# Optimization experiments

Hardware: AMD Instinct MI355X
Metric: run time of the kernel (lower is better)

## Reference

```python
import jax, jax.numpy as jnp
import numpy as np

BINS = 15
STEPS = 25
BETA = 0.8
THR = 1.0
ALPHA = 2.0  # snntorch surrogate.atan default
B = 131072
NUM_FEATURES = 4  # 60 / 15 bins


@jax.custom_vjp
def spike_fn(x):
    # Heaviside on shifted membrane (mem - threshold)
    return (x > 0).astype(x.dtype)


def _spike_fwd(x):
    return spike_fn(x), x


def _spike_bwd(x, g):
    # snntorch ATan surrogate gradient: alpha/2 / (1 + (pi/2 * alpha * x)^2)
    return (g * (ALPHA / 2) / (1 + (jnp.pi / 2 * ALPHA * x) ** 2),)


spike_fn.defvjp(_spike_fwd, _spike_bwd)


def population_encode(x, bins=BINS):
    # vectorized equivalent of the scalar double loop: one-hot bucketing per feature
    x = jnp.clip(x, 0.0, 1.0)
    idx = jnp.clip((x * (bins - 1)).astype(jnp.int32), 0, bins - 1)  # [B, F]
    bsz, nfeat = x.shape
    return jax.nn.one_hot(idx, bins, dtype=x.dtype).reshape(bsz, nfeat * bins)  # [B, F*bins]


def setup_inputs() -> dict:
    key = jax.random.key(0)
    k0, k1, k2, k3, k4 = jax.random.split(key, 5)
    x = jax.random.uniform(k0, (B, NUM_FEATURES), dtype=jnp.float32)
    # fc1: Linear(60, 64); fc2: Linear(64, 3). torch layout: W [out, in]
    s1 = 1.0 / np.sqrt(60.0)
    s2 = 1.0 / np.sqrt(64.0)
    W1 = jax.random.uniform(k1, (64, 60), jnp.float32, -s1, s1)
    b1 = jax.random.uniform(k2, (64,), jnp.float32, -s1, s1)
    W2 = jax.random.uniform(k3, (3, 64), jnp.float32, -s2, s2)
    b2 = jax.random.uniform(k4, (3,), jnp.float32, -s2, s2)
    return {"x": x, "W1": W1, "b1": b1, "W2": W2, "b2": b2}


def reference(x, W1, b1, W2, b2):
    x_pop = population_encode(x)                # [B, 60]
    cur1 = x_pop @ W1.T + b1                    # [B, 64]; constant over steps (fc1 recomputed on same input)
    mem1_0 = jnp.zeros_like(cur1)               # [B, 64]
    mem2_0 = jnp.zeros((x.shape[0], W2.shape[0]), cur1.dtype)  # [B, 3]

    def step(carry, _):
        mem1, mem2 = carry
        # snntorch Leaky: reset from spike of incoming mem (detached), then leak+integrate, then fire
        reset1 = jax.lax.stop_gradient((mem1 > THR).astype(mem1.dtype))
        mem1 = BETA * mem1 + cur1 - reset1 * THR
        spk1 = spike_fn(mem1 - THR)
        cur2 = spk1 @ W2.T + b2                 # [B, 3]
        reset2 = jax.lax.stop_gradient((mem2 > THR).astype(mem2.dtype))
        mem2 = BETA * mem2 + cur2 - reset2 * THR
        spk2 = spike_fn(mem2 - THR)
        return (mem1, mem2), (spk2, spk1)

    _, (spk2_rec, spk1_rec) = jax.lax.scan(step, (mem1_0, mem2_0), None, length=STEPS)
    return spk2_rec, spk1_rec, x_pop            # [25,B,3], [25,B,64], [B,60]
```

## Files before the change

### kernel.cpp

```cpp
#include <hip/hip_runtime.h>


#define BINS   15
#define STEPS  25
#define NH     64
#define NO     3
#define NF     4
#define TPB    256

typedef float f32x4 __attribute__((ext_vector_type(4)));

__global__ __launch_bounds__(TPB) void popnet_kernel(
                              const float* __restrict__ x,
                              const float* __restrict__ W1,
                              const float* __restrict__ b1,
                              const float* __restrict__ W2,
                              const float* __restrict__ b2,
                              float* __restrict__ out, int B)
{
    __shared__ float W1s[NH * 60];
    __shared__ float b1s[NH];
    __shared__ float W2s[NO * NH];
    __shared__ float b2s[NO];
    __shared__ unsigned long long s1bits[TPB];
    __shared__ float s2f[TPB * NO];
    __shared__ unsigned int idxs[TPB];

    const int tid = threadIdx.x;
    for (int i = tid; i < NH * 60; i += TPB) W1s[i] = W1[i];
    for (int i = tid; i < NH;      i += TPB) b1s[i] = b1[i];
    for (int i = tid; i < NO * NH; i += TPB) W2s[i] = W2[i];
    if (tid < NO) b2s[tid] = b2[tid];
    __syncthreads();

    const int blockStart = blockIdx.x * TPB;
    const int b = blockStart + tid;

    const f32x4 xv = *reinterpret_cast<const f32x4*>(x + (size_t)b * NF);
    int idx[NF];
#pragma unroll
    for (int f = 0; f < NF; ++f) {
        float v = fminf(fmaxf(xv[f], 0.0f), 1.0f);
        int id = (int)(v * 14.0f);
        id = min(max(id, 0), BINS - 1);
        idx[f] = id;
    }
    idxs[tid] = (unsigned)idx[0] | ((unsigned)idx[1] << 4) |
                ((unsigned)idx[2] << 8) | ((unsigned)idx[3] << 12);
    const int c0 = idx[0], c1 = 15 + idx[1], c2 = 30 + idx[2], c3 = 45 + idx[3];

    float cur1[NH];
#pragma unroll
    for (int o = 0; o < NH; ++o) {
        const float* row = W1s + o * 60;
        float s = __fadd_rn(__fadd_rn(__fadd_rn(row[c0], row[c1]), row[c2]), row[c3]);
        cur1[o] = __fadd_rn(s, b1s[o]);
    }

    float mem1[NH];
#pragma unroll
    for (int o = 0; o < NH; ++o) mem1[o] = 0.0f;
    float mem2[NO] = {0.0f, 0.0f, 0.0f};

    const size_t off1 = (size_t)STEPS * B * NO;
    const size_t off2 = off1 + (size_t)STEPS * B * NH;
    float* const out_spk2 = out;
    float* const out_spk1 = out + off1;
    float* const out_xpop = out + off2;

#pragma unroll 1
    for (int t = 0; t < STEPS; ++t) {
        float acc0 = 0.0f, acc1 = 0.0f, acc2 = 0.0f;
        unsigned long long bits = 0ull;
#pragma unroll
        for (int n = 0; n < NH; ++n) {
            float m = mem1[n];
            const float reset = (m > 1.0f) ? 1.0f : 0.0f;
            m = __fsub_rn(__fadd_rn(__fmul_rn(0.8f, m), cur1[n]), reset);
            mem1[n] = m;
            const bool fire = (m > 1.0f);
            bits |= ((unsigned long long)(fire ? 1u : 0u)) << n;
            acc0 = __fadd_rn(acc0, fire ? W2s[0 * NH + n] : 0.0f);
            acc1 = __fadd_rn(acc1, fire ? W2s[1 * NH + n] : 0.0f);
            acc2 = __fadd_rn(acc2, fire ? W2s[2 * NH + n] : 0.0f);
        }
        s1bits[tid] = bits;

        const float cu[NO] = {__fadd_rn(acc0, b2s[0]), __fadd_rn(acc1, b2s[1]), __fadd_rn(acc2, b2s[2])};
#pragma unroll
        for (int k = 0; k < NO; ++k) {
            float m = mem2[k];
            const float reset = (m > 1.0f) ? 1.0f : 0.0f;
            m = __fsub_rn(__fadd_rn(__fmul_rn(0.8f, m), cu[k]), reset);
            mem2[k] = m;
            s2f[tid * NO + k] = (m > 1.0f) ? 1.0f : 0.0f;
        }
        __syncthreads();

        float* const base1 = out_spk1 + (size_t)t * B * NH + (size_t)blockStart * NH;
#pragma unroll
        for (int i = 0; i < 16; ++i) {
            const int f4 = tid + i * TPB;
            const unsigned long long w = s1bits[f4 >> 4];
            const int n0 = (f4 & 15) * 4;
            f32x4 v;
            v.x = (float)((w >> (n0 + 0)) & 1ull);
            v.y = (float)((w >> (n0 + 1)) & 1ull);
            v.z = (float)((w >> (n0 + 2)) & 1ull);
            v.w = (float)((w >> (n0 + 3)) & 1ull);
            __builtin_nontemporal_store(v, reinterpret_cast<f32x4*>(base1) + f4);
        }
        float* const base2 = out_spk2 + (size_t)t * B * NO + (size_t)blockStart * NO;
        if (tid < (TPB * NO) / 4) {
            f32x4 v;
            v.x = s2f[tid * 4 + 0];
            v.y = s2f[tid * 4 + 1];
            v.z = s2f[tid * 4 + 2];
            v.w = s2f[tid * 4 + 3];
            __builtin_nontemporal_store(v, reinterpret_cast<f32x4*>(base2) + tid);
        }
        __syncthreads();
    }

    float* const basex = out_xpop + (size_t)blockStart * 60;
#pragma unroll
    for (int i = 0; i < 15; ++i) {
        const int g = tid + i * TPB;
        const int bb = g / 15;
        const int r = g - bb * 15;
        const unsigned pk = idxs[bb];
        const int j0 = r * 4;
        f32x4 v;
#pragma unroll
        for (int k = 0; k < 4; ++k) {
            const int j = j0 + k;
            const int feat = j / 15;
            const int bin = j - feat * 15;
            v[k] = (bin == (int)((pk >> (feat * 4)) & 15u)) ? 1.0f : 0.0f;
        }
        __builtin_nontemporal_store(v, reinterpret_cast<f32x4*>(basex) + g);
    }
}

extern "C" void kernel_launch(void* const* d_in, const int* in_sizes, int n_in,
                              void* d_out, int out_size, void* d_ws, size_t ws_size,
                              hipStream_t stream) {
    const float* x  = (const float*)d_in[0];
    const float* W1 = (const float*)d_in[1];
    const float* b1 = (const float*)d_in[2];
    const float* W2 = (const float*)d_in[3];
    const float* b2 = (const float*)d_in[4];
    float* out = (float*)d_out;
    const int B = in_sizes[0] / NF;
    popnet_kernel<<<B / TPB, TPB, 0, stream>>>(x, W1, b1, W2, b2, out, B);
}
```

Measured before the change: 909.5 us.

## Split spike computation and spk1 float expansion into two kernels via bitmask workspace

The compute kernel no longer expands hidden-layer spikes into floats inside its time loop. Instead it writes a 64-bit spike mask per sample per step to workspace, and writes output-layer spikes directly. A second grid-stride kernel reads the masks and writes the large spk1 float tensor with fully coalesced vector stores. This removes the per-step block barriers and shared-memory staging from the register-heavy recurrent loop, and asks for two blocks per SM. In exchange it adds a second launch, a mask round trip through memory, uncoalesced 12-byte spk2 stores, and possible register spilling under the tighter launch bound.

```diff
diff --git a/kernel.cpp b/kernel.cpp
--- a/kernel.cpp
+++ b/kernel.cpp
@@ -10,20 +10,19 @@
 
 typedef float f32x4 __attribute__((ext_vector_type(4)));
 
-__global__ __launch_bounds__(TPB) void popnet_kernel(
+__global__ __launch_bounds__(TPB, 2) void popnet_compute(
                               const float* __restrict__ x,
                               const float* __restrict__ W1,
                               const float* __restrict__ b1,
                               const float* __restrict__ W2,
                               const float* __restrict__ b2,
-                              float* __restrict__ out, int B)
+                              float* __restrict__ out,
+                              unsigned long long* __restrict__ masks, int B)
 {
     __shared__ float W1s[NH * 60];
     __shared__ float b1s[NH];
     __shared__ float W2s[NO * NH];
     __shared__ float b2s[NO];
-    __shared__ unsigned long long s1bits[TPB];
-    __shared__ float s2f[TPB * NO];
     __shared__ unsigned int idxs[TPB];
 
     const int tid = threadIdx.x;
@@ -62,11 +61,9 @@
     for (int o = 0; o < NH; ++o) mem1[o] = 0.0f;
     float mem2[NO] = {0.0f, 0.0f, 0.0f};
 
-    const size_t off1 = (size_t)STEPS * B * NO;
-    const size_t off2 = off1 + (size_t)STEPS * B * NH;
+    const size_t off2x = (size_t)STEPS * B * NO + (size_t)STEPS * B * NH;
     float* const out_spk2 = out;
-    float* const out_spk1 = out + off1;
-    float* const out_xpop = out + off2;
+    float* const out_xpop = out + off2x;
 
 #pragma unroll 1
     for (int t = 0; t < STEPS; ++t) {
@@ -84,43 +81,21 @@
             acc1 = __fadd_rn(acc1, fire ? W2s[1 * NH + n] : 0.0f);
             acc2 = __fadd_rn(acc2, fire ? W2s[2 * NH + n] : 0.0f);
         }
-        s1bits[tid] = bits;
+        masks[(size_t)t * B + b] = bits;
 
         const float cu[NO] = {__fadd_rn(acc0, b2s[0]), __fadd_rn(acc1, b2s[1]), __fadd_rn(acc2, b2s[2])};
+        float* const w2dst = out_spk2 + ((size_t)t * B + b) * NO;
 #pragma unroll
         for (int k = 0; k < NO; ++k) {
             float m = mem2[k];
             const float reset = (m > 1.0f) ? 1.0f : 0.0f;
             m = __fsub_rn(__fadd_rn(__fmul_rn(0.8f, m), cu[k]), reset);
             mem2[k] = m;
-            s2f[tid * NO + k] = (m > 1.0f) ? 1.0f : 0.0f;
+            w2dst[k] = (m > 1.0f) ? 1.0f : 0.0f;
         }
-        __syncthreads();
+    }
 
-        float* const base1 = out_spk1 + (size_t)t * B * NH + (size_t)blockStart * NH;
-#pragma unroll
-        for (int i = 0; i < 16; ++i) {
-            const int f4 = tid + i * TPB;
-            const unsigned long long w = s1bits[f4 >> 4];
-            const int n0 = (f4 & 15) * 4;
-            f32x4 v;
-            v.x = (float)((w >> (n0 + 0)) & 1ull);
-            v.y = (float)((w >> (n0 + 1)) & 1ull);
-            v.z = (float)((w >> (n0 + 2)) & 1ull);
-            v.w = (float)((w >> (n0 + 3)) & 1ull);
-            __builtin_nontemporal_store(v, reinterpret_cast<f32x4*>(base1) + f4);
-        }
-        float* const base2 = out_spk2 + (size_t)t * B * NO + (size_t)blockStart * NO;
-        if (tid < (TPB * NO) / 4) {
-            f32x4 v;
-            v.x = s2f[tid * 4 + 0];
-            v.y = s2f[tid * 4 + 1];
-            v.z = s2f[tid * 4 + 2];
-            v.w = s2f[tid * 4 + 3];
-            __builtin_nontemporal_store(v, reinterpret_cast<f32x4*>(base2) + tid);
-        }
-        __syncthreads();
-    }
+    __syncthreads();
 
     float* const basex = out_xpop + (size_t)blockStart * 60;
 #pragma unroll
@@ -138,7 +113,32 @@
             const int bin = j - feat * 15;
             v[k] = (bin == (int)((pk >> (feat * 4)) & 15u)) ? 1.0f : 0.0f;
         }
-        __builtin_nontemporal_store(v, reinterpret_cast<f32x4*>(basex) + g);
+        reinterpret_cast<f32x4*>(basex)[g] = v;
+    }
+}
+
+__global__ __launch_bounds__(TPB) void spk1_expand(
+                              const unsigned long long* __restrict__ masks,
+                              float* __restrict__ out_spk1, int B)
+{
+    const long long total = (long long)STEPS * B * 16;
+    const int per_shift = 31 - __clz(B * 16);
+    const long long stride = (long long)gridDim.x * TPB;
+    f32x4* const dst = reinterpret_cast<f32x4*>(out_spk1);
+
+    for (long long g = (long long)blockIdx.x * TPB + threadIdx.x; g < total; g += stride) {
+        const int t = (int)(g >> per_shift);
+        const int r = (int)(g & ((1ll << per_shift) - 1));
+        const int b = r >> 4;
+        const int q = r & 15;
+        const unsigned long long w = masks[(size_t)t * B + b];
+        const int n0 = q * 4;
+        f32x4 v;
+        v.x = (float)((w >> (n0 + 0)) & 1ull);
+        v.y = (float)((w >> (n0 + 1)) & 1ull);
+        v.z = (float)((w >> (n0 + 2)) & 1ull);
+        v.w = (float)((w >> (n0 + 3)) & 1ull);
+        dst[g] = v;
     }
 }
 
@@ -151,6 +151,11 @@
     const float* W2 = (const float*)d_in[3];
     const float* b2 = (const float*)d_in[4];
     float* out = (float*)d_out;
+    unsigned long long* masks = (unsigned long long*)d_ws;
     const int B = in_sizes[0] / NF;
-    popnet_kernel<<<B / TPB, TPB, 0, stream>>>(x, W1, b1, W2, b2, out, B);
+
+    popnet_compute<<<B / TPB, TPB, 0, stream>>>(x, W1, b1, W2, b2, out, masks, B);
+
+    float* out_spk1 = out + (size_t)STEPS * B * NO;
+    spk1_expand<<<2048, TPB, 0, stream>>>(masks, out_spk1, B);
 }
```

Measured after the change: 1.253 ms. 1.38x slower.

## Split each batch element across four lanes and drop per-step block barriers

Applied to the files above, without the earlier changes.

Each batch element is now handled by four threads, each owning 16 hidden neurons, so per-thread register state shrinks and the grid grows fourfold. The fc2 partial sums are combined with lane shuffles instead of shared-memory staging. Spike stores are written directly from registers, which removes both __syncthreads per timestep. The trade-off is more shuffle work per step and loss of the nontemporal store hints, and each block now loads the W1 table into shared memory for only 64 elements.

```diff
diff --git a/kernel.cpp b/kernel.cpp
--- a/kernel.cpp
+++ b/kernel.cpp
@@ -7,10 +7,11 @@
 #define NO     3
 #define NF     4
 #define TPB    256
+#define EPB    (TPB / 4)
 
 typedef float f32x4 __attribute__((ext_vector_type(4)));
 
-__global__ __launch_bounds__(TPB) void popnet_kernel(
+__global__ __launch_bounds__(TPB, 4) void popnet_kernel(
                               const float* __restrict__ x,
                               const float* __restrict__ W1,
                               const float* __restrict__ b1,
@@ -22,9 +23,7 @@
     __shared__ float b1s[NH];
     __shared__ float W2s[NO * NH];
     __shared__ float b2s[NO];
-    __shared__ unsigned long long s1bits[TPB];
-    __shared__ float s2f[TPB * NO];
-    __shared__ unsigned int idxs[TPB];
+    __shared__ unsigned int idxs[EPB];
 
     const int tid = threadIdx.x;
     for (int i = tid; i < NH * 60; i += TPB) W1s[i] = W1[i];
@@ -33,112 +32,120 @@
     if (tid < NO) b2s[tid] = b2[tid];
     __syncthreads();
 
-    const int blockStart = blockIdx.x * TPB;
-    const int b = blockStart + tid;
+    const int lane   = tid & 63;
+    const int q      = tid & 3;
+    const int eLocal = tid >> 2;
+    const int e      = blockIdx.x * EPB + eLocal;
+    const int lbase  = lane & ~3;
 
-    const f32x4 xv = *reinterpret_cast<const f32x4*>(x + (size_t)b * NF);
-    int idx[NF];
+    const float xq = x[(size_t)e * NF + q];
+    float v = fminf(fmaxf(xq, 0.0f), 1.0f);
+    int myid = (int)(v * 14.0f);
+    myid = min(max(myid, 0), BINS - 1);
+
+    int idx_f[NF];
 #pragma unroll
-    for (int f = 0; f < NF; ++f) {
-        float v = fminf(fmaxf(xv[f], 0.0f), 1.0f);
-        int id = (int)(v * 14.0f);
-        id = min(max(id, 0), BINS - 1);
-        idx[f] = id;
+    for (int f = 0; f < NF; ++f) idx_f[f] = __shfl(myid, lbase + f);
+    const int c0 = idx_f[0], c1 = 15 + idx_f[1], c2 = 30 + idx_f[2], c3 = 45 + idx_f[3];
+    if (q == 0)
+        idxs[eLocal] = (unsigned)idx_f[0] | ((unsigned)idx_f[1] << 4) |
+                       ((unsigned)idx_f[2] << 8) | ((unsigned)idx_f[3] << 12);
+
+    const int n0 = q * 16;
+    float w2r0[16], w2r1[16], w2r2[16], cur1[16], mem1[16];
+#pragma unroll
+    for (int j = 0; j < 16; ++j) {
+        const int n = n0 + j;
+        w2r0[j] = W2s[0 * NH + n];
+        w2r1[j] = W2s[1 * NH + n];
+        w2r2[j] = W2s[2 * NH + n];
+        const float* row = W1s + n * 60;
+        float s = __fadd_rn(__fadd_rn(__fadd_rn(row[c0], row[c1]), row[c2]), row[c3]);
+        cur1[j] = __fadd_rn(s, b1s[n]);
+        mem1[j] = 0.0f;
     }
-    idxs[tid] = (unsigned)idx[0] | ((unsigned)idx[1] << 4) |
-                ((unsigned)idx[2] << 8) | ((unsigned)idx[3] << 12);
-    const int c0 = idx[0], c1 = 15 + idx[1], c2 = 30 + idx[2], c3 = 45 + idx[3];
-
-    float cur1[NH];
-#pragma unroll
-    for (int o = 0; o < NH; ++o) {
-        const float* row = W1s + o * 60;
-        float s = __fadd_rn(__fadd_rn(__fadd_rn(row[c0], row[c1]), row[c2]), row[c3]);
-        cur1[o] = __fadd_rn(s, b1s[o]);
-    }
-
-    float mem1[NH];
-#pragma unroll
-    for (int o = 0; o < NH; ++o) mem1[o] = 0.0f;
     float mem2[NO] = {0.0f, 0.0f, 0.0f};
 
-    const size_t off1 = (size_t)STEPS * B * NO;
-    const size_t off2 = off1 + (size_t)STEPS * B * NH;
     float* const out_spk2 = out;
-    float* const out_spk1 = out + off1;
-    float* const out_xpop = out + off2;
+    float* const out_spk1 = out + (size_t)STEPS * B * NO;
+    float* const out_xpop = out + (size_t)STEPS * B * NO + (size_t)STEPS * B * NH;
 
 #pragma unroll 1
     for (int t = 0; t < STEPS; ++t) {
-        float acc0 = 0.0f, acc1 = 0.0f, acc2 = 0.0f;
-        unsigned long long bits = 0ull;
+        float sp[16];
 #pragma unroll
-        for (int n = 0; n < NH; ++n) {
-            float m = mem1[n];
+        for (int j = 0; j < 16; ++j) {
+            float m = mem1[j];
             const float reset = (m > 1.0f) ? 1.0f : 0.0f;
-            m = __fsub_rn(__fadd_rn(__fmul_rn(0.8f, m), cur1[n]), reset);
-            mem1[n] = m;
-            const bool fire = (m > 1.0f);
-            bits |= ((unsigned long long)(fire ? 1u : 0u)) << n;
-            acc0 = __fadd_rn(acc0, fire ? W2s[0 * NH + n] : 0.0f);
-            acc1 = __fadd_rn(acc1, fire ? W2s[1 * NH + n] : 0.0f);
-            acc2 = __fadd_rn(acc2, fire ? W2s[2 * NH + n] : 0.0f);
+            m = __fsub_rn(__fadd_rn(__fmul_rn(0.8f, m), cur1[j]), reset);
+            mem1[j] = m;
+            sp[j] = (m > 1.0f) ? 1.0f : 0.0f;
         }
-        s1bits[tid] = bits;
 
-        const float cu[NO] = {__fadd_rn(acc0, b2s[0]), __fadd_rn(acc1, b2s[1]), __fadd_rn(acc2, b2s[2])};
+        float* const dst = out_spk1 + ((size_t)t * B + e) * NH + n0;
+#pragma unroll
+        for (int j4 = 0; j4 < 4; ++j4) {
+            f32x4 vv;
+            vv.x = sp[j4 * 4 + 0];
+            vv.y = sp[j4 * 4 + 1];
+            vv.z = sp[j4 * 4 + 2];
+            vv.w = sp[j4 * 4 + 3];
+            reinterpret_cast<f32x4*>(dst)[j4] = vv;
+        }
+
+        float a0 = 0.0f, a1 = 0.0f, a2 = 0.0f;
+#pragma unroll
+        for (int p = 0; p < 4; ++p) {
+            const bool mine = (q == p);
+#pragma unroll
+            for (int j = 0; j < 16; ++j) {
+                const bool on = mine && (sp[j] != 0.0f);
+                a0 = __fadd_rn(a0, on ? w2r0[j] : 0.0f);
+                a1 = __fadd_rn(a1, on ? w2r1[j] : 0.0f);
+                a2 = __fadd_rn(a2, on ? w2r2[j] : 0.0f);
+            }
+            a0 = __shfl(a0, lbase + p);
+            a1 = __shfl(a1, lbase + p);
+            a2 = __shfl(a2, lbase + p);
+        }
+
+        const float cu[NO] = {__fadd_rn(a0, b2s[0]), __fadd_rn(a1, b2s[1]), __fadd_rn(a2, b2s[2])};
+        float s2[NO];
 #pragma unroll
         for (int k = 0; k < NO; ++k) {
             float m = mem2[k];
             const float reset = (m > 1.0f) ? 1.0f : 0.0f;
             m = __fsub_rn(__fadd_rn(__fmul_rn(0.8f, m), cu[k]), reset);
             mem2[k] = m;
-            s2f[tid * NO + k] = (m > 1.0f) ? 1.0f : 0.0f;
+            s2[k] = (m > 1.0f) ? 1.0f : 0.0f;
         }
-        __syncthreads();
-
-        float* const base1 = out_spk1 + (size_t)t * B * NH + (size_t)blockStart * NH;
-#pragma unroll
-        for (int i = 0; i < 16; ++i) {
-            const int f4 = tid + i * TPB;
-            const unsigned long long w = s1bits[f4 >> 4];
-            const int n0 = (f4 & 15) * 4;
-            f32x4 v;
-            v.x = (float)((w >> (n0 + 0)) & 1ull);
-            v.y = (float)((w >> (n0 + 1)) & 1ull);
-            v.z = (float)((w >> (n0 + 2)) & 1ull);
-            v.w = (float)((w >> (n0 + 3)) & 1ull);
-            __builtin_nontemporal_store(v, reinterpret_cast<f32x4*>(base1) + f4);
+        if (q < NO) {
+            const float mys2 = (q == 0) ? s2[0] : (q == 1) ? s2[1] : s2[2];
+            out_spk2[((size_t)t * B + e) * NO + q] = mys2;
         }
-        float* const base2 = out_spk2 + (size_t)t * B * NO + (size_t)blockStart * NO;
-        if (tid < (TPB * NO) / 4) {
-            f32x4 v;
-            v.x = s2f[tid * 4 + 0];
-            v.y = s2f[tid * 4 + 1];
-            v.z = s2f[tid * 4 + 2];
-            v.w = s2f[tid * 4 + 3];
-            __builtin_nontemporal_store(v, reinterpret_cast<f32x4*>(base2) + tid);
-        }
-        __syncthreads();
     }
 
-    float* const basex = out_xpop + (size_t)blockStart * 60;
+    __syncthreads();
+
+    float* const basex = out_xpop + (size_t)(blockIdx.x * EPB) * 60;
 #pragma unroll
-    for (int i = 0; i < 15; ++i) {
+    for (int i = 0; i < 4; ++i) {
         const int g = tid + i * TPB;
-        const int bb = g / 15;
-        const int r = g - bb * 15;
-        const unsigned pk = idxs[bb];
-        const int j0 = r * 4;
-        f32x4 v;
+        if (g < 960) {
+            const int el = g / 15;
+            const int r  = g - el * 15;
+            const unsigned pk = idxs[el];
+            const int j0 = r * 4;
+            f32x4 vv;
 #pragma unroll
-        for (int k = 0; k < 4; ++k) {
-            const int j = j0 + k;
-            const int feat = j / 15;
-            const int bin = j - feat * 15;
-            v[k] = (bin == (int)((pk >> (feat * 4)) & 15u)) ? 1.0f : 0.0f;
+            for (int k = 0; k < 4; ++k) {
+                const int j = j0 + k;
+                const int feat = j / 15;
+                const int bin  = j - feat * 15;
+                vv[k] = (bin == (int)((pk >> (feat * 4)) & 15u)) ? 1.0f : 0.0f;
+            }
+            reinterpret_cast<f32x4*>(basex)[g] = vv;
         }
-        __builtin_nontemporal_store(v, reinterpret_cast<f32x4*>(basex) + g);
     }
 }
 
@@ -152,5 +159,5 @@
     const float* b2 = (const float*)d_in[4];
     float* out = (float*)d_out;
     const int B = in_sizes[0] / NF;
-    popnet_kernel<<<B / TPB, TPB, 0, stream>>>(x, W1, b1, W2, b2, out, B);
+    popnet_kernel<<<B / EPB, TPB, 0, stream>>>(x, W1, b1, W2, b2, out, B);
 }
```

Result: slower. 990.1 us (+8.9%).
